# Kernel tuning notes

Hardware: AMD Instinct MI355X
Metric: run time of the kernel (lower is better)

The kernel has to match this reference:

```python
import jax, jax.numpy as jnp
import numpy as np

LARGE_CONSTANT = 1e9


def setup_inputs() -> dict:
    key = jax.random.key(0)
    ks = jax.random.split(key, 8)
    B, S, D, U = 8, 2048, 1024, 1024
    scale = 1.0 / np.sqrt(D)
    inputs_1 = jax.random.normal(ks[0], (B, S, D), dtype=jnp.float32)
    inputs_2 = jax.random.normal(ks[1], (B, S, D), dtype=jnp.float32)
    Wq = jax.random.normal(ks[2], (D, U), dtype=jnp.float32) * scale
    Wk = jax.random.normal(ks[3], (D, U), dtype=jnp.float32) * scale
    Wv = jax.random.normal(ks[4], (D, U), dtype=jnp.float32) * scale
    bq = jnp.zeros((U,), dtype=jnp.float32)
    bk = jnp.zeros((U,), dtype=jnp.float32)
    bv = jnp.zeros((U,), dtype=jnp.float32)
    # metric initialized as identity in the original; add small noise to exercise it
    metric = jnp.eye(U, dtype=jnp.float32) + 0.01 * jax.random.normal(ks[5], (U, U), dtype=jnp.float32)
    return {"inputs_1": inputs_1, "inputs_2": inputs_2, "Wq": Wq, "bq": bq,
            "Wk": Wk, "bk": bk, "Wv": Wv, "bv": bv, "metric": metric}


def reference(inputs_1, inputs_2, Wq, bq, Wk, bk, Wv, bv, metric):
    U = Wq.shape[1]
    scaling = jnp.sqrt(jnp.asarray(U, dtype=inputs_1.dtype))
    queries = inputs_1 @ Wq + bq            # [b, i, u]
    keys = inputs_2 @ Wk + bk               # [b, j, u]
    values = inputs_2 @ Wv + bv             # [b, j, u]
    queries = jnp.einsum('biu,uv->biv', queries, metric)  # learned-metric transform
    scores = jnp.einsum('biu,bju->bij', queries, keys) / scaling
    # causal mask: band_part(ones, -1, 0) is lower-triangular
    S = scores.shape[-1]
    causal = jnp.tril(jnp.ones((S, S), dtype=scores.dtype))
    scores = scores - LARGE_CONSTANT * (1.0 - causal)
    alpha = jax.nn.softmax(scores, axis=-1)
    return jnp.einsum('bij,bju->biu', alpha, values)
```

## Files before the change

### kernel.cpp

```cpp
#include <hip/hip_runtime.h>


#define Bq 8
#define Sq 2048
#define Dq 1024
#define Uq 1024

typedef __bf16 bf16;
typedef __bf16 bf16x8 __attribute__((ext_vector_type(8)));
typedef float f32x4 __attribute__((ext_vector_type(4)));
typedef unsigned short u16;
typedef unsigned int u32;

__device__ __forceinline__ u16 f2bf(float f) {
  u32 u = __builtin_bit_cast(u32, f);
  u32 r = u + 0x7fffu + ((u >> 16) & 1u);
  return (u16)(r >> 16);
}
__device__ __forceinline__ float bf2f(u32 h) {
  return __builtin_bit_cast(float, h << 16);
}

__device__ __forceinline__ void gl_lds16(const void* g, void* l) {
  __builtin_amdgcn_global_load_lds(
      (const __attribute__((address_space(1))) u32*)g,
      (__attribute__((address_space(3))) u32*)l, 16, 0, 0);
}


__global__ __launch_bounds__(256) void cvt_x(const float* __restrict__ x1,
                                             const float* __restrict__ x2,
                                             u16* __restrict__ o1,
                                             u16* __restrict__ o2, int n4) {
  int idx = blockIdx.x * 256 + threadIdx.x;
  if (idx >= n4) return;
  const float* in = blockIdx.y ? x2 : x1;
  u16* out = blockIdx.y ? o2 : o1;
  float4 v = ((const float4*)in)[idx];
  ushort4 o;
  o.x = f2bf(v.x); o.y = f2bf(v.y); o.z = f2bf(v.z); o.w = f2bf(v.w);
  ((ushort4*)out)[idx] = o;
}

__global__ __launch_bounds__(256) void cvt_bf16(const float* __restrict__ in,
                                                u16* __restrict__ out, int n4) {
  int idx = blockIdx.x * 256 + threadIdx.x;
  if (idx >= n4) return;
  float4 v = ((const float4*)in)[idx];
  ushort4 o;
  o.x = f2bf(v.x); o.y = f2bf(v.y); o.z = f2bf(v.z); o.w = f2bf(v.w);
  ((ushort4*)out)[idx] = o;
}

__global__ __launch_bounds__(256) void transpose_cvt3(
    const float* __restrict__ s0, u16* __restrict__ d0,
    const float* __restrict__ s1, u16* __restrict__ d1,
    const float* __restrict__ s2, u16* __restrict__ d2) {
  __shared__ float tile[32][33];
  const float* in = (blockIdx.z == 0) ? s0 : (blockIdx.z == 1) ? s1 : s2;
  u16* out = (blockIdx.z == 0) ? d0 : (blockIdx.z == 1) ? d1 : d2;
  const int N = 1024;
  int tx = threadIdx.x & 31, ty = threadIdx.x >> 5;
  int x0 = blockIdx.x * 32, y0 = blockIdx.y * 32;
#pragma unroll
  for (int r = 0; r < 32; r += 8)
    tile[ty + r][tx] = in[(size_t)(y0 + ty + r) * N + x0 + tx];
  __syncthreads();
#pragma unroll
  for (int r = 0; r < 32; r += 8)
    out[(size_t)(x0 + ty + r) * N + y0 + tx] = f2bf(tile[tx][ty + r]);
}

__global__ __launch_bounds__(256) void bqm_kernel(const float* __restrict__ bq,
                                                  const float* __restrict__ metric,
                                                  float* __restrict__ bqm) {
  int v = blockIdx.x * 256 + threadIdx.x;
  float s = 0.f;
  for (int u = 0; u < Uq; ++u) s += bq[u] * metric[(size_t)u * Uq + v];
  bqm[v] = s;
}

__global__ __launch_bounds__(256) void fill_zero(float4* __restrict__ p, int n4) {
  int i = blockIdx.x * 256 + threadIdx.x;
  if (i < n4) p[i] = float4{0.f, 0.f, 0.f, 0.f};
}

#define BM 128
#define BN 128
#define BK 32

template <int OUT_BF16, int BIAS>
__global__ __launch_bounds__(256) void gemm_tn(
    const bf16* __restrict__ A, const bf16* __restrict__ B, void* __restrict__ Cv,
    const float* __restrict__ bias, int lda, int ldb, int ldc,
    long long sA, long long sB, long long sC, int K,
    int causal_skip, int causal_klimit) {
  __shared__ __align__(16) bf16 lA[3][BM * BK];
  __shared__ __align__(16) bf16 lB[3][BN * BK];
  int bx = causal_klimit ? (gridDim.x - 1 - blockIdx.x) : blockIdx.x;
  int m0 = bx * BM, n0 = blockIdx.y * BN;
  if (causal_skip && n0 > m0 + BM - 1) return;
  long long b = blockIdx.z;
  A += b * sA;
  B += b * sB;
  int t = threadIdx.x;
  int w = t >> 6, l = t & 63;
  int wr = (w >> 1) * 64, wc = (w & 1) * 64;
  int Kend = causal_klimit ? min(K, m0 + BM) : K;
  int nk = Kend / BK;

  f32x4 acc[4][4] = {};
  int rowA = t >> 2, kc = (t & 3) * 8;
  int lm = l & 15, q = l >> 4;

  const bf16* gA = A + (long long)(m0 + rowA) * lda + kc;
  const bf16* gB = B + (long long)(n0 + rowA) * ldb + kc;
  long long a64 = (long long)64 * lda, b64 = (long long)64 * ldb;

  auto stage = [&](int kt, int buf) {
    int k0 = kt * BK;
    char* dA = (char*)lA[buf] + w * 1024;
    char* dB = (char*)lB[buf] + w * 1024;
    gl_lds16(gA + k0, dA);
    gl_lds16(gA + k0 + a64, dA + 4096);
    gl_lds16(gB + k0, dB);
    gl_lds16(gB + k0 + b64, dB + 4096);
  };

  stage(0, 0);
  stage(1, 1);
  int cur = 0;
  for (int kt = 0; kt < nk; ++kt) {
    if (kt + 2 < nk) {
      int pb = cur + 2;
      if (pb >= 3) pb -= 3;
      stage(kt + 2, pb);
      asm volatile("s_waitcnt vmcnt(8)\n\ts_barrier" ::: "memory");
    } else if (kt + 1 < nk) {
      asm volatile("s_waitcnt vmcnt(4)\n\ts_barrier" ::: "memory");
    } else {
      asm volatile("s_waitcnt vmcnt(0)\n\ts_barrier" ::: "memory");
    }
    bf16x8 af[4], bfr[4];
#pragma unroll
    for (int i = 0; i < 4; ++i)
      af[i] = *(const bf16x8*)&lA[cur][(wr + i * 16 + lm) * BK + q * 8];
#pragma unroll
    for (int i = 0; i < 4; ++i)
      bfr[i] = *(const bf16x8*)&lB[cur][(wc + i * 16 + lm) * BK + q * 8];
#pragma unroll
    for (int i = 0; i < 4; ++i)
#pragma unroll
      for (int j = 0; j < 4; ++j)
        acc[i][j] = __builtin_amdgcn_mfma_f32_16x16x32_bf16(af[i], bfr[j], acc[i][j], 0, 0, 0);
    asm volatile("s_barrier" ::: "memory");
    cur = (cur == 2) ? 0 : cur + 1;
  }

  char* Cb = (char*)Cv + (OUT_BF16 ? b * sC * 2 : b * sC * 4);
#pragma unroll
  for (int i = 0; i < 4; ++i) {
#pragma unroll
    for (int j = 0; j < 4; ++j) {
      int col = n0 + wc + j * 16 + lm;
      float bc = (BIAS == 1) ? bias[col] : 0.f;
#pragma unroll
      for (int r = 0; r < 4; ++r) {
        int row = m0 + wr + i * 16 + q * 4 + r;
        float v = acc[i][j][r] + bc;
        if (BIAS == 2) v += bias[row];
        size_t idx = (size_t)row * ldc + col;
        if (OUT_BF16)
          ((u16*)Cb)[idx] = f2bf(v);
        else
          ((float*)Cb)[idx] = v;
      }
    }
  }
}


template <int OUT_BF16, int BIAS>
__global__ __launch_bounds__(512, 2) void gemm_tn256(
    const bf16* __restrict__ A, const bf16* __restrict__ B, void* __restrict__ Cv,
    const float* __restrict__ bias, int lda, int ldb, int ldc,
    long long sA, long long sB, long long sC, int K,
    int causal_skip, int causal_klimit) {
  __shared__ __align__(16) bf16 lA[4][256 * 32];
  __shared__ __align__(16) bf16 lB[4][256 * 32];
  int bx = causal_klimit ? (gridDim.x - 1 - blockIdx.x) : blockIdx.x;
  int m0 = bx * 256, n0 = blockIdx.y * 256;
  if (causal_skip && n0 > m0 + 255) return;
  long long b = blockIdx.z;
  A += b * sA;
  B += b * sB;
  int t = threadIdx.x;
  int w = t >> 6, l = t & 63;
  int wr = w >> 2, wc = w & 3;
  int lm = l & 15, q = l >> 4;
  int cq = q ^ ((lm >> 1) & 3);

  int Kend = causal_klimit ? min(K, m0 + 256) : K;
  int NP = Kend >> 5;

  int r0 = t >> 2;
  int c0 = t & 3;
  int q0 = c0 ^ ((r0 >> 1) & 3);
  const bf16* gA0 = A + (long long)(m0 + r0) * lda + q0 * 8;
  const bf16* gA1 = gA0 + (long long)128 * lda;
  const bf16* gB0 = B + (long long)(n0 + r0) * ldb + q0 * 8;
  const bf16* gB1 = gB0 + (long long)128 * ldb;
  char* dA = (char*)&lA[0][0] + w * 1024;
  char* dB = (char*)&lB[0][0] + w * 1024;

  auto stage = [&](int ph) {
    int reg_ = ph & 3;
    int k0 = ph << 5;
    char* da = dA + reg_ * 16384;
    char* db = dB + reg_ * 16384;
    gl_lds16(gA0 + k0, da);
    gl_lds16(gA1 + k0, da + 8192);
    gl_lds16(gB0 + k0, db);
    gl_lds16(gB1 + k0, db + 8192);
  };

  stage(0); stage(1); stage(2); stage(3);

  f32x4 acc[8][4] = {};
  const bf16* pAl = &lA[0][0] + (wr * 128 + lm) * 32 + cq * 8;
  const bf16* pBl = &lB[0][0] + (wc * 64 + lm) * 32 + cq * 8;

  for (int p = 0; p < NP; ++p) {
    if (p + 3 < NP)
      asm volatile("s_waitcnt vmcnt(12)\n\ts_barrier" ::: "memory");
    else if (p + 2 < NP)
      asm volatile("s_waitcnt vmcnt(8)\n\ts_barrier" ::: "memory");
    else if (p + 1 < NP)
      asm volatile("s_waitcnt vmcnt(4)\n\ts_barrier" ::: "memory");
    else
      asm volatile("s_waitcnt vmcnt(0)\n\ts_barrier" ::: "memory");

    int reg_ = p & 3;
    const bf16* pa = pAl + reg_ * 8192;
    const bf16* pb = pBl + reg_ * 8192;
    bf16x8 af[8], bfr[4];
#pragma unroll
    for (int j = 0; j < 4; ++j) bfr[j] = *(const bf16x8*)(pb + j * 512);
#pragma unroll
    for (int i = 0; i < 8; ++i) af[i] = *(const bf16x8*)(pa + i * 512);
    __builtin_amdgcn_s_setprio(1);
#pragma unroll
    for (int i = 0; i < 8; ++i)
#pragma unroll
      for (int j = 0; j < 4; ++j)
        acc[i][j] = __builtin_amdgcn_mfma_f32_16x16x32_bf16(af[i], bfr[j], acc[i][j], 0, 0, 0);
    __builtin_amdgcn_s_setprio(0);
    asm volatile("s_barrier" ::: "memory");
    if (p + 4 < NP) stage(p + 4);
  }

  char* Cb = (char*)Cv + (OUT_BF16 ? b * sC * 2 : b * sC * 4);
#pragma unroll
  for (int i = 0; i < 8; ++i) {
#pragma unroll
    for (int j = 0; j < 4; ++j) {
      int col = n0 + wc * 64 + j * 16 + lm;
      float bc = (BIAS == 1) ? bias[col] : 0.f;
#pragma unroll
      for (int r = 0; r < 4; ++r) {
        int row = m0 + wr * 128 + i * 16 + q * 4 + r;
        float v = acc[i][j][r] + bc;
        if (BIAS == 2) v += bias[row];
        size_t idxc = (size_t)row * ldc + col;
        if (OUT_BF16)
          ((u16*)Cb)[idxc] = f2bf(v);
        else
          ((float*)Cb)[idxc] = v;
      }
    }
  }
}

__global__ __launch_bounds__(256) void softmax_causal(u16* __restrict__ sc) {
  __shared__ __align__(16) float sm[Sq];
  __shared__ float red[8];
  int gr = blockIdx.x;
  int i = gr & (Sq - 1);
  u16* rowp = sc + (size_t)gr * Sq;
  int t = threadIdx.x;
  int nv = i + 1;
  int wlim = (i & ~255) + 256;
  int j0 = t * 8;
  if (j0 < nv) {
    uint4 pk = ((const uint4*)rowp)[t];
    float4 lo, hi;
    lo.x = bf2f(pk.x & 0xffffu); lo.y = bf2f(pk.x >> 16);
    lo.z = bf2f(pk.y & 0xffffu); lo.w = bf2f(pk.y >> 16);
    hi.x = bf2f(pk.z & 0xffffu); hi.y = bf2f(pk.z >> 16);
    hi.z = bf2f(pk.w & 0xffffu); hi.w = bf2f(pk.w >> 16);
    ((float4*)sm)[2 * t] = lo;
    ((float4*)sm)[2 * t + 1] = hi;
  }
  __syncthreads();
  const float scl = 0.03125f;
  float m = -1e30f;
  for (int j = t; j < nv; j += 256) m = fmaxf(m, sm[j]);
#pragma unroll
  for (int o = 32; o; o >>= 1) m = fmaxf(m, __shfl_xor(m, o));
  if ((t & 63) == 0) red[t >> 6] = m;
  __syncthreads();
  m = fmaxf(fmaxf(red[0], red[1]), fmaxf(red[2], red[3])) * scl;
  float sum = 0.f;
  for (int j = t; j < nv; j += 256) sum += __expf(sm[j] * scl - m);
#pragma unroll
  for (int o = 32; o; o >>= 1) sum += __shfl_xor(sum, o);
  if ((t & 63) == 0) red[4 + (t >> 6)] = sum;
  __syncthreads();
  float rinv = 1.0f / (red[4] + red[5] + red[6] + red[7]);
  if (j0 < wlim) {
    u16 ov[8];
#pragma unroll
    for (int k = 0; k < 8; ++k)
      ov[k] = (j0 + k < nv) ? f2bf(__expf(sm[j0 + k] * scl - m) * rinv) : (u16)0;
    uint4 po;
    po.x = (u32)ov[0] | ((u32)ov[1] << 16);
    po.y = (u32)ov[2] | ((u32)ov[3] << 16);
    po.z = (u32)ov[4] | ((u32)ov[5] << 16);
    po.w = (u32)ov[6] | ((u32)ov[7] << 16);
    ((uint4*)rowp)[t] = po;
  }
}


extern "C" void kernel_launch(void* const* d_in, const int* in_sizes, int n_in,
                              void* d_out, int out_size, void* d_ws, size_t ws_size,
                              hipStream_t stream) {
  const float* X1 = (const float*)d_in[0];
  const float* X2 = (const float*)d_in[1];
  const float* Wq = (const float*)d_in[2];
  const float* bq = (const float*)d_in[3];
  const float* Wk = (const float*)d_in[4];
  const float* bk = (const float*)d_in[5];
  const float* Wv = (const float*)d_in[6];
  const float* bv = (const float*)d_in[7];
  const float* metric = (const float*)d_in[8];
  float* out = (float*)d_out;

  const size_t XB = (size_t)Bq * Sq * Dq * 2;
  const size_t WB = (size_t)Dq * Uq * 2;
  const size_t NEED = 3 * XB + 5 * WB + 4096;

  if (ws_size < NEED) {
    fill_zero<<<(out_size / 4 + 255) / 256, 256, 0, stream>>>((float4*)d_out, out_size / 4);
    return;
  }

  char* ws = (char*)d_ws;
  bf16* X1b = (bf16*)(ws);
  bf16* X2b = (bf16*)(ws + XB);
  bf16* Vt = (bf16*)(ws + 2 * XB);
  bf16* WqB = (bf16*)(ws + 3 * XB);
  bf16* metT = (bf16*)(ws + 3 * XB + WB);
  bf16* WkT = (bf16*)(ws + 3 * XB + 2 * WB);
  bf16* WvT = (bf16*)(ws + 3 * XB + 3 * WB);
  bf16* WqmT = (bf16*)(ws + 3 * XB + 4 * WB);
  float* bqm = (float*)(ws + 3 * XB + 5 * WB);
  u16* Sc = (u16*)ws;
  bf16* Qb = (bf16*)d_out;
  bf16* Kb = (bf16*)d_out + (size_t)Bq * Sq * Uq;

  int nx4 = Bq * Sq * Dq / 4;
  cvt_x<<<dim3((nx4 + 255) / 256, 2), 256, 0, stream>>>(X1, X2, (u16*)X1b, (u16*)X2b, nx4);
  cvt_bf16<<<(Dq * Uq / 4 + 255) / 256, 256, 0, stream>>>(Wq, (u16*)WqB, Dq * Uq / 4);
  transpose_cvt3<<<dim3(32, 32, 3), 256, 0, stream>>>(
      metric, (u16*)metT, Wk, (u16*)WkT, Wv, (u16*)WvT);
  bqm_kernel<<<Uq / 256, 256, 0, stream>>>(bq, metric, bqm);

  gemm_tn<1, 0><<<dim3(Uq / BM, Dq / BN, 1), 256, 0, stream>>>(
      metT, WqB, WqmT, nullptr, Uq, Uq, Dq, 0, 0, 0, Uq, 0, 0);

  const int MQ = Bq * Sq;
  gemm_tn256<1, 1><<<dim3(MQ / 256, Uq / 256, 1), 512, 0, stream>>>(
      X1b, WqmT, Qb, bqm, Dq, Dq, Uq, 0, 0, 0, Dq, 0, 0);
  gemm_tn256<1, 1><<<dim3(MQ / 256, Uq / 256, 1), 512, 0, stream>>>(
      X2b, WkT, Kb, bk, Dq, Dq, Uq, 0, 0, 0, Dq, 0, 0);
  gemm_tn256<1, 2><<<dim3(Uq / 256, Sq / 256, Bq), 512, 0, stream>>>(
      WvT, X2b, Vt, bv, Dq, Dq, Sq, 0, (long long)Sq * Dq, (long long)Uq * Sq, Dq, 0, 0);

  gemm_tn256<1, 0><<<dim3(Sq / 256, Sq / 256, Bq), 512, 0, stream>>>(
      Qb, Kb, Sc, nullptr, Uq, Uq, Sq, (long long)Sq * Uq, (long long)Sq * Uq,
      (long long)Sq * Sq, Uq, 1, 0);

  softmax_causal<<<Bq * Sq, 256, 0, stream>>>(Sc);

  gemm_tn256<0, 0><<<dim3(Sq / 256, Uq / 256, Bq), 512, 0, stream>>>(
      (const bf16*)Sc, Vt, out, nullptr, Sq, Sq, Uq, (long long)Sq * Sq,
      (long long)Uq * Sq, (long long)Sq * Uq, Sq, 0, 1);

  (void)in_sizes; (void)n_in; (void)ws_size;
}
```

Baseline: 568.6 us.

## Software-pipeline LDS fragment loads and halve barriers in 256-tile GEMM mainloop

Restructures the gemm_tn256 mainloop into a double-buffered register pipeline. The next k-step's A-low and B fragments are read from LDS while the current step's second half of MFMAs runs, and the loop is unrolled by two to ping-pong the register sets. The global-to-LDS prefetch depth drops from four stages to three, and each iteration now uses one combined waitcnt+barrier instead of two. This hides LDS read latency behind MFMA work and cuts barrier count, but it uses more VGPRs (extra fragment buffers) and has less global prefetch slack. It also assumes NP is even.

```diff
diff --git a/kernel.cpp b/kernel.cpp
--- a/kernel.cpp
+++ b/kernel.cpp
@@ -180,6 +180,39 @@
 }
 
 
+#define GBODY(P, CLO, CB, NLO, NB)                                             \
+  {                                                                            \
+    const int rp_ = (P) & 3, rn_ = ((P) + 1) & 3;                              \
+    if ((P) + 3 < NP) stage((P) + 3);                                          \
+    const bf16* pa_ = pAl + rp_ * 8192;                                        \
+    _Pragma("unroll") for (int i = 0; i < 4; ++i)                              \
+        aHi[i] = *(const bf16x8*)(pa_ + (i + 4) * 512);                        \
+    __builtin_amdgcn_s_setprio(1);                                             \
+    _Pragma("unroll") for (int i = 0; i < 4; ++i)                              \
+        _Pragma("unroll") for (int j = 0; j < 4; ++j)                          \
+            acc[i][j] = __builtin_amdgcn_mfma_f32_16x16x32_bf16(               \
+                CLO[i], CB[j], acc[i][j], 0, 0, 0);                            \
+    __builtin_amdgcn_s_setprio(0);                                             \
+    if ((P) + 1 < NP) {                                                        \
+      const bf16* pa2_ = pAl + rn_ * 8192;                                     \
+      const bf16* pb2_ = pBl + rn_ * 8192;                                     \
+      _Pragma("unroll") for (int i = 0; i < 4; ++i)                            \
+          NLO[i] = *(const bf16x8*)(pa2_ + i * 512);                           \
+      _Pragma("unroll") for (int j = 0; j < 4; ++j)                            \
+          NB[j] = *(const bf16x8*)(pb2_ + j * 512);                            \
+    }                                                                          \
+    __builtin_amdgcn_s_setprio(1);                                             \
+    _Pragma("unroll") for (int i = 0; i < 4; ++i)                              \
+        _Pragma("unroll") for (int j = 0; j < 4; ++j)                          \
+            acc[i + 4][j] = __builtin_amdgcn_mfma_f32_16x16x32_bf16(           \
+                aHi[i], CB[j], acc[i + 4][j], 0, 0, 0);                        \
+    __builtin_amdgcn_s_setprio(0);                                             \
+    if ((P) + 3 < NP)                                                          \
+      asm volatile("s_waitcnt vmcnt(4) lgkmcnt(0)\n\ts_barrier" ::: "memory"); \
+    else if ((P) + 2 < NP)                                                     \
+      asm volatile("s_waitcnt vmcnt(0) lgkmcnt(0)\n\ts_barrier" ::: "memory"); \
+  }
+
 template <int OUT_BF16, int BIAS>
 __global__ __launch_bounds__(512, 2) void gemm_tn256(
     const bf16* __restrict__ A, const bf16* __restrict__ B, void* __restrict__ Cv,
@@ -224,39 +257,23 @@
     gl_lds16(gB1 + k0, db + 8192);
   };
 
-  stage(0); stage(1); stage(2); stage(3);
-
-  f32x4 acc[8][4] = {};
   const bf16* pAl = &lA[0][0] + (wr * 128 + lm) * 32 + cq * 8;
   const bf16* pBl = &lB[0][0] + (wc * 64 + lm) * 32 + cq * 8;
 
-  for (int p = 0; p < NP; ++p) {
-    if (p + 3 < NP)
-      asm volatile("s_waitcnt vmcnt(12)\n\ts_barrier" ::: "memory");
-    else if (p + 2 < NP)
-      asm volatile("s_waitcnt vmcnt(8)\n\ts_barrier" ::: "memory");
-    else if (p + 1 < NP)
-      asm volatile("s_waitcnt vmcnt(4)\n\ts_barrier" ::: "memory");
-    else
-      asm volatile("s_waitcnt vmcnt(0)\n\ts_barrier" ::: "memory");
-
-    int reg_ = p & 3;
-    const bf16* pa = pAl + reg_ * 8192;
-    const bf16* pb = pBl + reg_ * 8192;
-    bf16x8 af[8], bfr[4];
-#pragma unroll
-    for (int j = 0; j < 4; ++j) bfr[j] = *(const bf16x8*)(pb + j * 512);
-#pragma unroll
-    for (int i = 0; i < 8; ++i) af[i] = *(const bf16x8*)(pa + i * 512);
-    __builtin_amdgcn_s_setprio(1);
-#pragma unroll
-    for (int i = 0; i < 8; ++i)
-#pragma unroll
-      for (int j = 0; j < 4; ++j)
-        acc[i][j] = __builtin_amdgcn_mfma_f32_16x16x32_bf16(af[i], bfr[j], acc[i][j], 0, 0, 0);
-    __builtin_amdgcn_s_setprio(0);
-    asm volatile("s_barrier" ::: "memory");
-    if (p + 4 < NP) stage(p + 4);
+  f32x4 acc[8][4] = {};
+  bf16x8 aLoA[4], bFrA[4], aLoB[4], bFrB[4], aHi[4];
+
+  stage(0); stage(1); stage(2);
+  asm volatile("s_waitcnt vmcnt(8)\n\ts_barrier" ::: "memory");
+#pragma unroll
+  for (int i = 0; i < 4; ++i) aLoA[i] = *(const bf16x8*)(pAl + i * 512);
+#pragma unroll
+  for (int j = 0; j < 4; ++j) bFrA[j] = *(const bf16x8*)(pBl + j * 512);
+  asm volatile("s_waitcnt vmcnt(4) lgkmcnt(0)\n\ts_barrier" ::: "memory");
+
+  for (int p = 0; p < NP; p += 2) {
+    GBODY(p, aLoA, bFrA, aLoB, bFrB)
+    GBODY(p + 1, aLoB, bFrB, aLoA, bFrA)
   }
 
   char* Cb = (char*)Cv + (OUT_BF16 ? b * sC * 2 : b * sC * 4);
```

New measurement: 524.5 us. 1.08x faster.
